# Performance work log

Hardware: AMD Instinct MI355X
Metric: run time of the kernel (lower is better)

Reference implementation:

```python
import jax, jax.numpy as jnp
import numpy as np

N = 262144        # input_size = n_nodes * in_features (n_kernels = 1)
E = 16777216      # number of nonzero (i, j, param_idx) entries in weight_distribution
NPARAMS = 1280    # in_features * n_node_labels^2 * max_distance * n_kernels
NB = 16           # in_features * n_node_labels * n_kernels


def setup_inputs() -> dict:
    key = jax.random.key(0)
    ks = jax.random.split(key, 7)
    return {
        "x": jax.random.normal(ks[0], (N,), jnp.float32),
        "Param_W": jax.random.normal(ks[1], (NPARAMS,), jnp.float32),
        "Param_b": jax.random.normal(ks[2], (NB,), jnp.float32),
        "w_rows": jax.random.randint(ks[3], (E,), 0, N, jnp.int32),
        "w_cols": jax.random.randint(ks[4], (E,), 0, N, jnp.int32),
        "w_params": jax.random.randint(ks[5], (E,), 0, NPARAMS, jnp.int32),
        "b_params": jax.random.randint(ks[6], (N,), 0, NB, jnp.int32),
    }


def reference(x, Param_W, Param_b, w_rows, w_cols, w_params, b_params):
    # Original: W[i, j] = Param_W[p] for every (i, j, p) in weight_distribution,
    # then out = W @ x + bias. Fused gather-scale-scatter avoids materializing W.
    vals = Param_W[w_params] * x[w_cols]              # [E]
    out = jax.ops.segment_sum(vals, w_rows, num_segments=N)  # [N]
    # bias[i] = Param_b[b_params[i]] (one shared bias per output position)
    return out + Param_b[b_params]
```

## Files before the change

### kernel.cpp

```cpp
#include <hip/hip_runtime.h>


#define SLICE_BITS   15
#define SLICE_SIZE   (1 << SLICE_BITS)
#define SLICES       8
#define CHUNKS       32
#define SCAN_THREADS 1024
#define BATCH        4
#define NPARAMS_MAX  2048

__global__ __launch_bounds__(SCAN_THREADS, 1) void slice_scan_kernel(
    const float* __restrict__ x, const float* __restrict__ PW, int nparams,
    const int4* __restrict__ rows4, const int4* __restrict__ cols4,
    const int4* __restrict__ params4, float* __restrict__ partials,
    int e4_per_chunk)
{
    __shared__ float acc[SLICE_SIZE];
    __shared__ float pw_lds[NPARAMS_MAX];
    const int bid = blockIdx.x;
    const int s = bid / CHUNKS;
    const int c = bid % CHUNKS;
    for (int j = threadIdx.x; j < SLICE_SIZE; j += SCAN_THREADS) acc[j] = 0.0f;
    for (int j = threadIdx.x; j < nparams; j += SCAN_THREADS) pw_lds[j] = PW[j];
    __syncthreads();

    const int4* rp = rows4   + (size_t)c * e4_per_chunk;
    const int4* cp = cols4   + (size_t)c * e4_per_chunk;
    const int4* qp = params4 + (size_t)c * e4_per_chunk;
    const int per_thread = e4_per_chunk / SCAN_THREADS;

    for (int base = 0; base < per_thread; base += BATCH) {
        int4 r[BATCH], cc[BATCH], pp[BATCH];
#pragma unroll
        for (int b = 0; b < BATCH; ++b) {
            const int g = (base + b) * SCAN_THREADS + threadIdx.x;
            r[b]  = rp[g];
            cc[b] = cp[g];
            pp[b] = qp[g];
        }
#pragma unroll
        for (int b = 0; b < BATCH; ++b) {
            if ((r[b].x >> SLICE_BITS) == s)
                atomicAdd(&acc[r[b].x & (SLICE_SIZE - 1)], pw_lds[pp[b].x] * x[cc[b].x]);
            if ((r[b].y >> SLICE_BITS) == s)
                atomicAdd(&acc[r[b].y & (SLICE_SIZE - 1)], pw_lds[pp[b].y] * x[cc[b].y]);
            if ((r[b].z >> SLICE_BITS) == s)
                atomicAdd(&acc[r[b].z & (SLICE_SIZE - 1)], pw_lds[pp[b].z] * x[cc[b].z]);
            if ((r[b].w >> SLICE_BITS) == s)
                atomicAdd(&acc[r[b].w & (SLICE_SIZE - 1)], pw_lds[pp[b].w] * x[cc[b].w]);
        }
    }
    __syncthreads();

    float* dst = partials + (size_t)bid * SLICE_SIZE;
    for (int j = threadIdx.x; j < SLICE_SIZE; j += SCAN_THREADS) dst[j] = acc[j];
}

__global__ __launch_bounds__(256) void reduce_bias_kernel(
    const float* __restrict__ partials, const float* __restrict__ Pb,
    const int* __restrict__ bp, float* __restrict__ out, int n)
{
    const int i = blockIdx.x * 256 + threadIdx.x;
    if (i >= n) return;
    const int s = i >> SLICE_BITS;
    const int j = i & (SLICE_SIZE - 1);
    const float* p = partials + ((size_t)s * CHUNKS) * SLICE_SIZE + j;
    float sum = 0.0f;
#pragma unroll
    for (int g = 0; g < CHUNKS; ++g) sum += p[(size_t)g * SLICE_SIZE];
    out[i] = sum + Pb[bp[i]];
}


__global__ __launch_bounds__(256) void bias_init_kernel(const float* __restrict__ Pb,
                                                        const int* __restrict__ bp,
                                                        float* __restrict__ out, int n) {
    int i = blockIdx.x * 256 + threadIdx.x;
    if (i < n) out[i] = Pb[bp[i]];
}

__global__ __launch_bounds__(256) void edge_scatter_kernel(const float* __restrict__ x,
                                                           const float* __restrict__ PW,
                                                           const int* __restrict__ rows,
                                                           const int* __restrict__ cols,
                                                           const int* __restrict__ params,
                                                           float* __restrict__ out, int E) {
    int e = blockIdx.x * 256 + threadIdx.x;
    if (e < E) atomicAdd(out + rows[e], PW[params[e]] * x[cols[e]]);
}

extern "C" void kernel_launch(void* const* d_in, const int* in_sizes, int n_in,
                              void* d_out, int out_size, void* d_ws, size_t ws_size,
                              hipStream_t stream) {
    const float* x        = (const float*)d_in[0];
    const float* Param_W  = (const float*)d_in[1];
    const float* Param_b  = (const float*)d_in[2];
    const int*   w_rows   = (const int*)d_in[3];
    const int*   w_cols   = (const int*)d_in[4];
    const int*   w_params = (const int*)d_in[5];
    const int*   b_params = (const int*)d_in[6];
    float* out = (float*)d_out;

    const int N_  = in_sizes[0];
    const int NP_ = in_sizes[1];
    const int E_  = in_sizes[3];

    const size_t ws_needed = (size_t)SLICES * CHUNKS * SLICE_SIZE * sizeof(float);
    const bool shape_ok = (N_ == SLICES * SLICE_SIZE) &&
                          (E_ % (4 * CHUNKS * SCAN_THREADS * BATCH) == 0) &&
                          (NP_ <= NPARAMS_MAX);

    if (shape_ok && ws_size >= ws_needed) {
        float* partials = (float*)d_ws;
        const int e4_per_chunk = E_ / 4 / CHUNKS;
        slice_scan_kernel<<<SLICES * CHUNKS, SCAN_THREADS, 0, stream>>>(
            x, Param_W, NP_, (const int4*)w_rows, (const int4*)w_cols,
            (const int4*)w_params, partials, e4_per_chunk);
        reduce_bias_kernel<<<(N_ + 255) / 256, 256, 0, stream>>>(
            partials, Param_b, b_params, out, N_);
    } else {
        bias_init_kernel<<<(N_ + 255) / 256, 256, 0, stream>>>(Param_b, b_params, out, N_);
        edge_scatter_kernel<<<(E_ + 255) / 256, 256, 0, stream>>>(
            x, Param_W, w_rows, w_cols, w_params, out, E_);
    }
}
```

Baseline: 368.5 us.

## Bucket edges by row slice before LDS accumulation instead of rescanning per slice

Replaces the per-slice rescan, where every one of 8 slices re-reads all edge arrays, with a two-pass scheme. A scatter kernel first computes the edge values and writes (row, value) pairs bucketed by slice, using per-block histograms and wave-aggregated cursors. An accumulate kernel then reads only its own slice's pairs into an LDS accumulator. This cuts edge-array reads from 8 passes to one, at the cost of writing and re-reading a large intermediate buffer. When the workspace is too small, it falls back to a packed 4-byte bf16-rounded pair format, which loses precision.

Result: slower. 449.6 us (+22.0%).

```diff
diff --git a/kernel.cpp b/kernel.cpp
--- a/kernel.cpp
+++ b/kernel.cpp
@@ -1,15 +1,159 @@
 #include <hip/hip_runtime.h>
 
 
-#define SLICE_BITS   15
-#define SLICE_SIZE   (1 << SLICE_BITS)
-#define SLICES       8
-#define CHUNKS       32
-#define SCAN_THREADS 1024
-#define BATCH        4
-#define NPARAMS_MAX  2048
-
-__global__ __launch_bounds__(SCAN_THREADS, 1) void slice_scan_kernel(
+#define SLICE_BITS  15
+#define SLICE_SIZE  (1 << SLICE_BITS)
+#define SLICES      8
+#define ACC_CHUNKS  32
+#define NPARAMS_MAX 2048
+
+#define SC_BLOCKS   1024
+#define SC_THREADS  256
+#define EPB         16384
+#define GPB         (EPB / 4)
+#define TILES       8
+#define TILE_G      (GPB / TILES)
+
+template<bool PACKED>
+__global__ __launch_bounds__(SC_THREADS) void scatter_kernel(
+    const float* __restrict__ x, const float* __restrict__ PW, int nparams,
+    const int4* __restrict__ rows4, const int4* __restrict__ cols4,
+    const int4* __restrict__ params4,
+    void* __restrict__ pairs_v, int* __restrict__ ofs)
+{
+    __shared__ float pw_lds[NPARAMS_MAX];
+    __shared__ int ihist[8];
+    __shared__ int sbase[8];
+    __shared__ int cursor[8];
+
+    const int blk = blockIdx.x;
+    const int tid = threadIdx.x;
+    if (tid < 8) ihist[tid] = 0;
+    for (int j = tid; j < nparams; j += SC_THREADS) pw_lds[j] = PW[j];
+    __syncthreads();
+
+    const int4* rp = rows4   + (size_t)blk * GPB;
+    const int4* cp = cols4   + (size_t)blk * GPB;
+    const int4* pp = params4 + (size_t)blk * GPB;
+
+    unsigned long long c64 = 0;
+#pragma unroll
+    for (int i = 0; i < GPB / SC_THREADS; ++i) {
+        const int4 r = rp[i * SC_THREADS + tid];
+        c64 += 1ULL << ((r.x >> SLICE_BITS) * 8);
+        c64 += 1ULL << ((r.y >> SLICE_BITS) * 8);
+        c64 += 1ULL << ((r.z >> SLICE_BITS) * 8);
+        c64 += 1ULL << ((r.w >> SLICE_BITS) * 8);
+    }
+#pragma unroll
+    for (int b = 0; b < 8; ++b) {
+        const int c = (int)((c64 >> (b * 8)) & 0xFF);
+        if (c) atomicAdd(&ihist[b], c);
+    }
+    __syncthreads();
+    if (tid == 0) {
+        int run = 0;
+#pragma unroll
+        for (int b = 0; b < 8; ++b) { sbase[b] = run; cursor[b] = run; run += ihist[b]; }
+    }
+    __syncthreads();
+    if (tid < 8) ofs[blk * 8 + tid] = sbase[tid];
+
+    const int lane = tid & 63;
+    const unsigned long long lt = (1ULL << lane) - 1ULL;
+
+    for (int t = 0; t < TILES; ++t) {
+        const int g0 = t * TILE_G + tid;
+        const int g1 = g0 + SC_THREADS;
+        const int4 r0 = rp[g0], r1 = rp[g1];
+        const int4 c0 = cp[g0], c1 = cp[g1];
+        const int4 p0 = pp[g0], p1 = pp[g1];
+        const int e[8]  = { r0.x, r0.y, r0.z, r0.w, r1.x, r1.y, r1.z, r1.w };
+        const int cc[8] = { c0.x, c0.y, c0.z, c0.w, c1.x, c1.y, c1.z, c1.w };
+        const int pq[8] = { p0.x, p0.y, p0.z, p0.w, p1.x, p1.y, p1.z, p1.w };
+        float v[8];
+#pragma unroll
+        for (int j = 0; j < 8; ++j) v[j] = pw_lds[pq[j]] * x[cc[j]];
+#pragma unroll
+        for (int j = 0; j < 8; ++j) {
+            const int b   = e[j] >> SLICE_BITS;
+            const int r15 = e[j] & (SLICE_SIZE - 1);
+#pragma unroll
+            for (int B = 0; B < 8; ++B) {
+                const unsigned long long m = __ballot(b == B);
+                if (m == 0) continue;
+                const int leader = __ffsll((unsigned long long)m) - 1;
+                int base = 0;
+                if (lane == leader) base = atomicAdd(&cursor[B], __popcll(m));
+                base = __shfl(base, leader);
+                if (b == B) {
+                    const size_t dst = (size_t)blk * EPB + base + __popcll(m & lt);
+                    if (PACKED) {
+                        const unsigned int u =
+                            (__float_as_uint(v[j]) + 0x8000u) & 0xFFFF0000u;
+                        ((unsigned int*)pairs_v)[dst] = u | (unsigned int)r15;
+                    } else {
+                        ((int2*)pairs_v)[dst] = make_int2(r15, __float_as_int(v[j]));
+                    }
+                }
+            }
+        }
+    }
+}
+
+template<bool PACKED>
+__global__ __launch_bounds__(1024, 1) void accum_kernel(
+    const void* __restrict__ pairs_v, const int* __restrict__ ofs,
+    float* __restrict__ partials)
+{
+    __shared__ float acc[SLICE_SIZE];
+    const int B = blockIdx.x >> 5;
+    const int k = blockIdx.x & 31;
+    for (int j = threadIdx.x; j < SLICE_SIZE; j += 1024) acc[j] = 0.0f;
+    __syncthreads();
+    for (int blk = k * 32; blk < k * 32 + 32; ++blk) {
+        const int o   = ofs[blk * 8 + B];
+        const int end = (B == 7) ? EPB : ofs[blk * 8 + B + 1];
+        const size_t base = (size_t)blk * EPB;
+        if (PACKED) {
+            const unsigned int* p = (const unsigned int*)pairs_v;
+            for (int i = o + (int)threadIdx.x; i < end; i += 1024) {
+                const unsigned int u = p[base + i];
+                atomicAdd(&acc[u & (SLICE_SIZE - 1)], __uint_as_float(u & 0xFFFF0000u));
+            }
+        } else {
+            const int2* p = (const int2*)pairs_v;
+            for (int i = o + (int)threadIdx.x; i < end; i += 1024) {
+                const int2 q = p[base + i];
+                atomicAdd(&acc[q.x], __int_as_float(q.y));
+            }
+        }
+    }
+    __syncthreads();
+    float* dst = partials + (size_t)blockIdx.x * SLICE_SIZE;
+    for (int j = threadIdx.x; j < SLICE_SIZE; j += 1024) dst[j] = acc[j];
+}
+
+__global__ __launch_bounds__(256) void reduce_bias_kernel(
+    const float* __restrict__ partials, const float* __restrict__ Pb,
+    const int* __restrict__ bp, float* __restrict__ out, int n)
+{
+    const int i = blockIdx.x * 256 + threadIdx.x;
+    if (i >= n) return;
+    const int s = i >> SLICE_BITS;
+    const int j = i & (SLICE_SIZE - 1);
+    const float* p = partials + ((size_t)s * ACC_CHUNKS) * SLICE_SIZE + j;
+    float sum = 0.0f;
+#pragma unroll
+    for (int g = 0; g < ACC_CHUNKS; ++g) sum += p[(size_t)g * SLICE_SIZE];
+    out[i] = sum + Pb[bp[i]];
+}
+
+#define FB_CHUNKS 32
+#define FB_THREADS 1024
+#define FB_BATCH 4
+
+__global__ __launch_bounds__(FB_THREADS, 1) void slice_scan_kernel(
     const float* __restrict__ x, const float* __restrict__ PW, int nparams,
     const int4* __restrict__ rows4, const int4* __restrict__ cols4,
     const int4* __restrict__ params4, float* __restrict__ partials,
@@ -18,28 +162,24 @@
     __shared__ float acc[SLICE_SIZE];
     __shared__ float pw_lds[NPARAMS_MAX];
     const int bid = blockIdx.x;
-    const int s = bid / CHUNKS;
-    const int c = bid % CHUNKS;
-    for (int j = threadIdx.x; j < SLICE_SIZE; j += SCAN_THREADS) acc[j] = 0.0f;
-    for (int j = threadIdx.x; j < nparams; j += SCAN_THREADS) pw_lds[j] = PW[j];
-    __syncthreads();
-
+    const int s = bid / FB_CHUNKS;
+    const int c = bid % FB_CHUNKS;
+    for (int j = threadIdx.x; j < SLICE_SIZE; j += FB_THREADS) acc[j] = 0.0f;
+    for (int j = threadIdx.x; j < nparams; j += FB_THREADS) pw_lds[j] = PW[j];
+    __syncthreads();
     const int4* rp = rows4   + (size_t)c * e4_per_chunk;
     const int4* cp = cols4   + (size_t)c * e4_per_chunk;
     const int4* qp = params4 + (size_t)c * e4_per_chunk;
-    const int per_thread = e4_per_chunk / SCAN_THREADS;
-
-    for (int base = 0; base < per_thread; base += BATCH) {
-        int4 r[BATCH], cc[BATCH], pp[BATCH];
-#pragma unroll
-        for (int b = 0; b < BATCH; ++b) {
-            const int g = (base + b) * SCAN_THREADS + threadIdx.x;
-            r[b]  = rp[g];
-            cc[b] = cp[g];
-            pp[b] = qp[g];
-        }
-#pragma unroll
-        for (int b = 0; b < BATCH; ++b) {
+    const int per_thread = e4_per_chunk / FB_THREADS;
+    for (int base = 0; base < per_thread; base += FB_BATCH) {
+        int4 r[FB_BATCH], cc[FB_BATCH], pp[FB_BATCH];
+#pragma unroll
+        for (int b = 0; b < FB_BATCH; ++b) {
+            const int g = (base + b) * FB_THREADS + threadIdx.x;
+            r[b] = rp[g]; cc[b] = cp[g]; pp[b] = qp[g];
+        }
+#pragma unroll
+        for (int b = 0; b < FB_BATCH; ++b) {
             if ((r[b].x >> SLICE_BITS) == s)
                 atomicAdd(&acc[r[b].x & (SLICE_SIZE - 1)], pw_lds[pp[b].x] * x[cc[b].x]);
             if ((r[b].y >> SLICE_BITS) == s)
@@ -51,26 +191,9 @@
         }
     }
     __syncthreads();
-
     float* dst = partials + (size_t)bid * SLICE_SIZE;
-    for (int j = threadIdx.x; j < SLICE_SIZE; j += SCAN_THREADS) dst[j] = acc[j];
-}
-
-__global__ __launch_bounds__(256) void reduce_bias_kernel(
-    const float* __restrict__ partials, const float* __restrict__ Pb,
-    const int* __restrict__ bp, float* __restrict__ out, int n)
-{
-    const int i = blockIdx.x * 256 + threadIdx.x;
-    if (i >= n) return;
-    const int s = i >> SLICE_BITS;
-    const int j = i & (SLICE_SIZE - 1);
-    const float* p = partials + ((size_t)s * CHUNKS) * SLICE_SIZE + j;
-    float sum = 0.0f;
-#pragma unroll
-    for (int g = 0; g < CHUNKS; ++g) sum += p[(size_t)g * SLICE_SIZE];
-    out[i] = sum + Pb[bp[i]];
-}
-
+    for (int j = threadIdx.x; j < SLICE_SIZE; j += FB_THREADS) dst[j] = acc[j];
+}
 
 __global__ __launch_bounds__(256) void bias_init_kernel(const float* __restrict__ Pb,
                                                         const int* __restrict__ bp,
@@ -105,15 +228,39 @@
     const int NP_ = in_sizes[1];
     const int E_  = in_sizes[3];
 
-    const size_t ws_needed = (size_t)SLICES * CHUNKS * SLICE_SIZE * sizeof(float);
-    const bool shape_ok = (N_ == SLICES * SLICE_SIZE) &&
-                          (E_ % (4 * CHUNKS * SCAN_THREADS * BATCH) == 0) &&
-                          (NP_ <= NPARAMS_MAX);
-
-    if (shape_ok && ws_size >= ws_needed) {
+    const size_t partial_bytes = (size_t)SLICES * ACC_CHUNKS * SLICE_SIZE * sizeof(float);
+    const size_t ofs_bytes     = (size_t)SC_BLOCKS * 8 * sizeof(int);
+    const bool shapes_ok = (N_ == SLICES * SLICE_SIZE) && (E_ == SC_BLOCKS * EPB) &&
+                           (NP_ <= NPARAMS_MAX);
+    const size_t need_fp32   = (size_t)E_ * 8 + ofs_bytes + partial_bytes;
+    const size_t need_packed = (size_t)E_ * 4 + ofs_bytes + partial_bytes;
+
+    if (shapes_ok && ws_size >= need_fp32) {
+        void* pairs    = d_ws;
+        int*  ofs      = (int*)((char*)d_ws + (size_t)E_ * 8);
+        float* partials = (float*)((char*)d_ws + (size_t)E_ * 8 + ofs_bytes);
+        scatter_kernel<false><<<SC_BLOCKS, SC_THREADS, 0, stream>>>(
+            x, Param_W, NP_, (const int4*)w_rows, (const int4*)w_cols,
+            (const int4*)w_params, pairs, ofs);
+        accum_kernel<false><<<SLICES * ACC_CHUNKS, 1024, 0, stream>>>(pairs, ofs, partials);
+        reduce_bias_kernel<<<(N_ + 255) / 256, 256, 0, stream>>>(
+            partials, Param_b, b_params, out, N_);
+    } else if (shapes_ok && ws_size >= need_packed) {
+        void* pairs    = d_ws;
+        int*  ofs      = (int*)((char*)d_ws + (size_t)E_ * 4);
+        float* partials = (float*)((char*)d_ws + (size_t)E_ * 4 + ofs_bytes);
+        scatter_kernel<true><<<SC_BLOCKS, SC_THREADS, 0, stream>>>(
+            x, Param_W, NP_, (const int4*)w_rows, (const int4*)w_cols,
+            (const int4*)w_params, pairs, ofs);
+        accum_kernel<true><<<SLICES * ACC_CHUNKS, 1024, 0, stream>>>(pairs, ofs, partials);
+        reduce_bias_kernel<<<(N_ + 255) / 256, 256, 0, stream>>>(
+            partials, Param_b, b_params, out, N_);
+    } else if ((N_ == SLICES * SLICE_SIZE) &&
+               (E_ % (4 * FB_CHUNKS * FB_THREADS * FB_BATCH) == 0) &&
+               (NP_ <= NPARAMS_MAX) && ws_size >= partial_bytes) {
         float* partials = (float*)d_ws;
-        const int e4_per_chunk = E_ / 4 / CHUNKS;
-        slice_scan_kernel<<<SLICES * CHUNKS, SCAN_THREADS, 0, stream>>>(
+        const int e4_per_chunk = E_ / 4 / FB_CHUNKS;
+        slice_scan_kernel<<<SLICES * FB_CHUNKS, FB_THREADS, 0, stream>>>(
             x, Param_W, NP_, (const int4*)w_rows, (const int4*)w_cols,
             (const int4*)w_params, partials, e4_per_chunk);
         reduce_bias_kernel<<<(N_ + 255) / 256, 256, 0, stream>>>(
```

## Precompute edge values once, then slice-scan rows with branchless LDS atomics

Applied to the files above, without the earlier changes.

Adds a separate pass that computes each edge value PW[p]*x[col] exactly once and writes it to workspace. The slice scan then reads only rows and values. Before, each of the 8 slice blocks re-read cols and params and gathered x for its matching edges. Out-of-slice atomics are redirected to a per-thread dummy LDS slot so the atomic path has no branch. This costs an extra 64MB write plus reread of the values array, and every edge now performs an LDS atomic, including non-matching ones.

New measurement: 901.4 us. 145% more time.

```diff
diff --git a/kernel.cpp b/kernel.cpp
--- a/kernel.cpp
+++ b/kernel.cpp
@@ -1,14 +1,101 @@
 #include <hip/hip_runtime.h>
 
 
-#define SLICE_BITS   15
-#define SLICE_SIZE   (1 << SLICE_BITS)
-#define SLICES       8
-#define CHUNKS       32
+#define SLICE_BITS  15
+#define SLICE_SIZE  (1 << SLICE_BITS)
+#define SLICES      8
+#define CHUNKS      32
+#define NPARAMS_MAX 2048
 #define SCAN_THREADS 1024
-#define BATCH        4
-#define NPARAMS_MAX  2048
-
+#define SB          8
+#define VB          4
+
+__global__ __launch_bounds__(256) void val_kernel(
+    const float* __restrict__ x, const float* __restrict__ PW, int nparams,
+    const int4* __restrict__ cols4, const int4* __restrict__ params4,
+    float4* __restrict__ vals4)
+{
+    __shared__ float pw[NPARAMS_MAX];
+    for (int j = threadIdx.x; j < nparams; j += 256) pw[j] = PW[j];
+    __syncthreads();
+    const int base = blockIdx.x * (256 * VB) + threadIdx.x;
+    int4 c[VB], p[VB];
+#pragma unroll
+    for (int k = 0; k < VB; ++k) {
+        c[k] = cols4[base + k * 256];
+        p[k] = params4[base + k * 256];
+    }
+#pragma unroll
+    for (int k = 0; k < VB; ++k) {
+        float4 v;
+        v.x = pw[p[k].x] * x[c[k].x];
+        v.y = pw[p[k].y] * x[c[k].y];
+        v.z = pw[p[k].z] * x[c[k].z];
+        v.w = pw[p[k].w] * x[c[k].w];
+        vals4[base + k * 256] = v;
+    }
+}
+
+__global__ __launch_bounds__(SCAN_THREADS, 1) void scan2_kernel(
+    const int4* __restrict__ rows4, const float4* __restrict__ vals4,
+    float* __restrict__ partials, int e4_per_chunk)
+{
+    __shared__ float acc[SLICE_SIZE + SCAN_THREADS];
+    const int bid = blockIdx.x;
+    const int s = bid / CHUNKS;
+    const int c = bid % CHUNKS;
+    for (int j = threadIdx.x; j < SLICE_SIZE + SCAN_THREADS; j += SCAN_THREADS)
+        acc[j] = 0.0f;
+    __syncthreads();
+
+    const int dummy = SLICE_SIZE + threadIdx.x;
+    const int4*   rp = rows4 + (size_t)c * e4_per_chunk;
+    const float4* vp = vals4 + (size_t)c * e4_per_chunk;
+    const int per_thread = e4_per_chunk / SCAN_THREADS;
+
+    for (int base = 0; base < per_thread; base += SB) {
+        int4   r[SB];
+        float4 v[SB];
+#pragma unroll
+        for (int b = 0; b < SB; ++b) {
+            const int g = (base + b) * SCAN_THREADS + threadIdx.x;
+            r[b] = rp[g];
+            v[b] = vp[g];
+        }
+#pragma unroll
+        for (int b = 0; b < SB; ++b) {
+            const int ix = ((r[b].x >> SLICE_BITS) == s) ? (r[b].x & (SLICE_SIZE - 1)) : dummy;
+            const int iy = ((r[b].y >> SLICE_BITS) == s) ? (r[b].y & (SLICE_SIZE - 1)) : dummy;
+            const int iz = ((r[b].z >> SLICE_BITS) == s) ? (r[b].z & (SLICE_SIZE - 1)) : dummy;
+            const int iw = ((r[b].w >> SLICE_BITS) == s) ? (r[b].w & (SLICE_SIZE - 1)) : dummy;
+            atomicAdd(&acc[ix], v[b].x);
+            atomicAdd(&acc[iy], v[b].y);
+            atomicAdd(&acc[iz], v[b].z);
+            atomicAdd(&acc[iw], v[b].w);
+        }
+    }
+    __syncthreads();
+
+    float* dst = partials + (size_t)bid * SLICE_SIZE;
+    for (int j = threadIdx.x; j < SLICE_SIZE; j += SCAN_THREADS) dst[j] = acc[j];
+}
+
+__global__ __launch_bounds__(256) void reduce_bias_kernel(
+    const float* __restrict__ partials, const float* __restrict__ Pb,
+    const int* __restrict__ bp, float* __restrict__ out, int n)
+{
+    const int i = blockIdx.x * 256 + threadIdx.x;
+    if (i >= n) return;
+    const int s = i >> SLICE_BITS;
+    const int j = i & (SLICE_SIZE - 1);
+    const float* p = partials + ((size_t)s * CHUNKS) * SLICE_SIZE + j;
+    float sum = 0.0f;
+#pragma unroll
+    for (int g = 0; g < CHUNKS; ++g) sum += p[(size_t)g * SLICE_SIZE];
+    out[i] = sum + Pb[bp[i]];
+}
+
+#define FB_BATCH 4
 __global__ __launch_bounds__(SCAN_THREADS, 1) void slice_scan_kernel(
     const float* __restrict__ x, const float* __restrict__ PW, int nparams,
     const int4* __restrict__ rows4, const int4* __restrict__ cols4,
@@ -23,23 +110,19 @@
     for (int j = threadIdx.x; j < SLICE_SIZE; j += SCAN_THREADS) acc[j] = 0.0f;
     for (int j = threadIdx.x; j < nparams; j += SCAN_THREADS) pw_lds[j] = PW[j];
     __syncthreads();
-
     const int4* rp = rows4   + (size_t)c * e4_per_chunk;
     const int4* cp = cols4   + (size_t)c * e4_per_chunk;
     const int4* qp = params4 + (size_t)c * e4_per_chunk;
     const int per_thread = e4_per_chunk / SCAN_THREADS;
-
-    for (int base = 0; base < per_thread; base += BATCH) {
-        int4 r[BATCH], cc[BATCH], pp[BATCH];
-#pragma unroll
-        for (int b = 0; b < BATCH; ++b) {
+    for (int base = 0; base < per_thread; base += FB_BATCH) {
+        int4 r[FB_BATCH], cc[FB_BATCH], pp[FB_BATCH];
+#pragma unroll
+        for (int b = 0; b < FB_BATCH; ++b) {
             const int g = (base + b) * SCAN_THREADS + threadIdx.x;
-            r[b]  = rp[g];
-            cc[b] = cp[g];
-            pp[b] = qp[g];
-        }
-#pragma unroll
-        for (int b = 0; b < BATCH; ++b) {
+            r[b] = rp[g]; cc[b] = cp[g]; pp[b] = qp[g];
+        }
+#pragma unroll
+        for (int b = 0; b < FB_BATCH; ++b) {
             if ((r[b].x >> SLICE_BITS) == s)
                 atomicAdd(&acc[r[b].x & (SLICE_SIZE - 1)], pw_lds[pp[b].x] * x[cc[b].x]);
             if ((r[b].y >> SLICE_BITS) == s)
@@ -51,26 +134,9 @@
         }
     }
     __syncthreads();
-
     float* dst = partials + (size_t)bid * SLICE_SIZE;
     for (int j = threadIdx.x; j < SLICE_SIZE; j += SCAN_THREADS) dst[j] = acc[j];
 }
-
-__global__ __launch_bounds__(256) void reduce_bias_kernel(
-    const float* __restrict__ partials, const float* __restrict__ Pb,
-    const int* __restrict__ bp, float* __restrict__ out, int n)
-{
-    const int i = blockIdx.x * 256 + threadIdx.x;
-    if (i >= n) return;
-    const int s = i >> SLICE_BITS;
-    const int j = i & (SLICE_SIZE - 1);
-    const float* p = partials + ((size_t)s * CHUNKS) * SLICE_SIZE + j;
-    float sum = 0.0f;
-#pragma unroll
-    for (int g = 0; g < CHUNKS; ++g) sum += p[(size_t)g * SLICE_SIZE];
-    out[i] = sum + Pb[bp[i]];
-}
-
 
 __global__ __launch_bounds__(256) void bias_init_kernel(const float* __restrict__ Pb,
                                                         const int* __restrict__ bp,
@@ -104,15 +170,29 @@
     const int N_  = in_sizes[0];
     const int NP_ = in_sizes[1];
     const int E_  = in_sizes[3];
-
-    const size_t ws_needed = (size_t)SLICES * CHUNKS * SLICE_SIZE * sizeof(float);
-    const bool shape_ok = (N_ == SLICES * SLICE_SIZE) &&
-                          (E_ % (4 * CHUNKS * SCAN_THREADS * BATCH) == 0) &&
-                          (NP_ <= NPARAMS_MAX);
-
-    if (shape_ok && ws_size >= ws_needed) {
+    const int e4  = E_ / 4;
+
+    const size_t partial_bytes = (size_t)SLICES * CHUNKS * SLICE_SIZE * sizeof(float);
+    const size_t vals_bytes    = (size_t)E_ * sizeof(float);
+    const bool shapes_ok = (N_ == SLICES * SLICE_SIZE) && (NP_ <= NPARAMS_MAX) &&
+                           (E_ % (4 * 256 * VB) == 0) &&
+                           (E_ % (4 * CHUNKS * SCAN_THREADS * SB) == 0);
+
+    if (shapes_ok && ws_size >= vals_bytes + partial_bytes) {
+        float*  vals     = (float*)d_ws;
+        float*  partials = (float*)((char*)d_ws + vals_bytes);
+        const int e4_per_chunk = e4 / CHUNKS;
+        val_kernel<<<e4 / (256 * VB), 256, 0, stream>>>(
+            x, Param_W, NP_, (const int4*)w_cols, (const int4*)w_params, (float4*)vals);
+        scan2_kernel<<<SLICES * CHUNKS, SCAN_THREADS, 0, stream>>>(
+            (const int4*)w_rows, (const float4*)vals, partials, e4_per_chunk);
+        reduce_bias_kernel<<<(N_ + 255) / 256, 256, 0, stream>>>(
+            partials, Param_b, b_params, out, N_);
+    } else if ((N_ == SLICES * SLICE_SIZE) && (NP_ <= NPARAMS_MAX) &&
+               (E_ % (4 * CHUNKS * SCAN_THREADS * FB_BATCH) == 0) &&
+               ws_size >= partial_bytes) {
         float* partials = (float*)d_ws;
-        const int e4_per_chunk = E_ / 4 / CHUNKS;
+        const int e4_per_chunk = e4 / CHUNKS;
         slice_scan_kernel<<<SLICES * CHUNKS, SCAN_THREADS, 0, stream>>>(
             x, Param_W, NP_, (const int4*)w_rows, (const int4*)w_cols,
             (const int4*)w_params, partials, e4_per_chunk);
```
